# Kernel optimization log

Hardware: AMD Instinct MI355X
Metric: run time of the kernel (lower is better)

## Reference

```python
import jax, jax.numpy as jnp
import numpy as np

CHANNELS = 96


def make_sharpen_kernel(channels: int) -> jnp.ndarray:
    # (C_out, C_in, 3, 3), block-diagonal: per-channel 3x3 sharpen stencil
    k = jnp.full((3, 3), -0.1, dtype=jnp.float32).at[1, 1].set(1.8)
    eye = jnp.eye(channels, dtype=jnp.float32)  # (C, C)
    return eye[:, :, None, None] * k[None, None, :, :]


def setup_inputs() -> dict:
    key = jax.random.key(0)
    x = jax.random.normal(key, (16, CHANNELS, 256, 256), dtype=jnp.float32)
    kernel = make_sharpen_kernel(CHANNELS)
    return {"x": x, "kernel": kernel}


def reference(x, kernel):
    # Faithful to F.conv2d(x, kernel, stride=1, padding=1) with the dense
    # (block-diagonal) kernel the torch module constructs.
    return jax.lax.conv_general_dilated(
        x, kernel,
        window_strides=(1, 1),
        padding=((1, 1), (1, 1)),
        dimension_numbers=("NCHW", "OIHW", "NCHW"),
    )
```

## Files before the change

kernel.cpp:

```cpp
#include <hip/hip_runtime.h>

#define CHN 96
#define IMG_H 256
#define IMG_W 256
#define STRIP 64
#define WPB 8
#define GRP 8

typedef float vfloat4 __attribute__((ext_vector_type(4)));

struct Row { float l, x, y, z, w, r; };

__device__ __forceinline__ Row mkrow(vfloat4 v, int lane) {
    Row r;
    r.x = v.x; r.y = v.y; r.z = v.z; r.w = v.w;
    r.l = __shfl_up(v.w, 1);
    r.r = __shfl_down(v.x, 1);
    if (lane == 0)  r.l = 0.f;
    if (lane == 63) r.r = 0.f;
    return r;
}

__device__ __forceinline__ vfloat4 ldrow(const float* xp, int yy, int col) {
    if (yy < IMG_H)
        return __builtin_nontemporal_load(
            (const vfloat4*)(xp + (size_t)yy * IMG_W + col));
    return (vfloat4){0.f, 0.f, 0.f, 0.f};
}

__device__ __forceinline__ vfloat4 stencil(const Row& a, const Row& b, const Row& c,
                                           float w0, float w1, float w2,
                                           float w3, float w4, float w5,
                                           float w6, float w7, float w8) {
    vfloat4 o;
    o.x = w0*a.l + w1*a.x + w2*a.y
        + w3*b.l + w4*b.x + w5*b.y
        + w6*c.l + w7*c.x + w8*c.y;
    o.y = w0*a.x + w1*a.y + w2*a.z
        + w3*b.x + w4*b.y + w5*b.z
        + w6*c.x + w7*c.y + w8*c.z;
    o.z = w0*a.y + w1*a.z + w2*a.w
        + w3*b.y + w4*b.z + w5*b.w
        + w6*c.y + w7*c.z + w8*c.w;
    o.w = w0*a.z + w1*a.w + w2*a.r
        + w3*b.z + w4*b.w + w5*b.r
        + w6*c.z + w7*c.w + w8*c.r;
    return o;
}

__global__ __launch_bounds__(WPB * 64)
void sharpen3x3_pipe(const float* __restrict__ x,
                     const float* __restrict__ kern,
                     float* __restrict__ out)
{
    const int lane = threadIdx.x & 63;
    const int wave = threadIdx.x >> 6;

    const int strip_id = blockIdx.x * WPB + wave;
    const int spp      = IMG_H / STRIP;
    const int plane    = strip_id / spp;
    const int sy       = (strip_id % spp) * STRIP;
    const int c        = plane % CHN;

    const float* kw = kern + ((size_t)c * CHN + c) * 9;
    const float w0 = kw[0], w1 = kw[1], w2 = kw[2];
    const float w3 = kw[3], w4 = kw[4], w5 = kw[5];
    const float w6 = kw[6], w7 = kw[7], w8 = kw[8];

    const float* xp = x   + (size_t)plane * IMG_H * IMG_W;
    float*       op = out + (size_t)plane * IMG_H * IMG_W;

    const int col = 4 * lane;

    Row prev, cur;
    if (sy == 0) {
        prev = Row{0.f, 0.f, 0.f, 0.f, 0.f, 0.f};
    } else {
        prev = mkrow(ldrow(xp, sy - 1, col), lane);
    }
    cur = mkrow(ldrow(xp, sy, col), lane);

    vfloat4 va[GRP];
    #pragma unroll
    for (int j = 0; j < GRP; ++j) va[j] = ldrow(xp, sy + 1 + j, col);

    #pragma unroll 1
    for (int g = 0; g < STRIP / GRP; ++g) {
        const int y = sy + g * GRP;

        vfloat4 vb[GRP];
        if (g + 1 < STRIP / GRP) {
            #pragma unroll
            for (int j = 0; j < GRP; ++j)
                vb[j] = ldrow(xp, y + GRP + 1 + j, col);
        } else {
            #pragma unroll
            for (int j = 0; j < GRP; ++j)
                vb[j] = (vfloat4){0.f, 0.f, 0.f, 0.f};
        }

        #pragma unroll
        for (int j = 0; j < GRP; ++j) {
            Row n = mkrow(va[j], lane);
            vfloat4 o = stencil(prev, cur, n,
                                w0,w1,w2,w3,w4,w5,w6,w7,w8);
            __builtin_nontemporal_store(
                o, (vfloat4*)(op + (size_t)(y + j) * IMG_W + col));
            prev = cur;
            cur  = n;
        }

        #pragma unroll
        for (int j = 0; j < GRP; ++j) va[j] = vb[j];
    }
}

extern "C" void kernel_launch(void* const* d_in, const int* in_sizes, int n_in,
                              void* d_out, int out_size, void* d_ws, size_t ws_size,
                              hipStream_t stream) {
    const float* x    = (const float*)d_in[0];
    const float* kern = (const float*)d_in[1];
    float* out        = (float*)d_out;

    const int n_strips = 16 * CHN * (IMG_H / STRIP);
    const int grid     = n_strips / WPB;

    hipLaunchKernelGGL(sharpen3x3_pipe, dim3(grid), dim3(WPB * 64),
                       0, stream, x, kern, out);
}
```

Before: 153.8 us.

## Factor sharpen stencil into separable box sum plus center term

Replaces the nine-weight stencil with a horizontal three-tap sum per row. The three row sums are added, scaled by the shared neighbour weight, and a center correction term is added. This cuts the FMA count and register pressure. The single-buffered 8-row prefetch becomes a ping-pong of two 4-row buffers, and the launch bounds now ask for a minimum occupancy. The algebraic form assumes all eight off-center weights equal kw[0], which holds only for this sharpen kernel construction.

New measurement: 162.6 us. 1.06x slower.

```diff
diff --git a/kernel.cpp b/kernel.cpp
--- a/kernel.cpp
+++ b/kernel.cpp
@@ -5,21 +5,10 @@
 #define IMG_W 256
 #define STRIP 64
 #define WPB 8
-#define GRP 8
+#define GRP 4
+#define NG (STRIP / GRP)
 
 typedef float vfloat4 __attribute__((ext_vector_type(4)));
-
-struct Row { float l, x, y, z, w, r; };
-
-__device__ __forceinline__ Row mkrow(vfloat4 v, int lane) {
-    Row r;
-    r.x = v.x; r.y = v.y; r.z = v.z; r.w = v.w;
-    r.l = __shfl_up(v.w, 1);
-    r.r = __shfl_down(v.x, 1);
-    if (lane == 0)  r.l = 0.f;
-    if (lane == 63) r.r = 0.f;
-    return r;
-}
 
 __device__ __forceinline__ vfloat4 ldrow(const float* xp, int yy, int col) {
     if (yy < IMG_H)
@@ -28,28 +17,41 @@
     return (vfloat4){0.f, 0.f, 0.f, 0.f};
 }
 
-__device__ __forceinline__ vfloat4 stencil(const Row& a, const Row& b, const Row& c,
-                                           float w0, float w1, float w2,
-                                           float w3, float w4, float w5,
-                                           float w6, float w7, float w8) {
-    vfloat4 o;
-    o.x = w0*a.l + w1*a.x + w2*a.y
-        + w3*b.l + w4*b.x + w5*b.y
-        + w6*c.l + w7*c.x + w8*c.y;
-    o.y = w0*a.x + w1*a.y + w2*a.z
-        + w3*b.x + w4*b.y + w5*b.z
-        + w6*c.x + w7*c.y + w8*c.z;
-    o.z = w0*a.y + w1*a.z + w2*a.w
-        + w3*b.y + w4*b.z + w5*b.w
-        + w6*c.y + w7*c.z + w8*c.w;
-    o.w = w0*a.z + w1*a.w + w2*a.r
-        + w3*b.z + w4*b.w + w5*b.r
-        + w6*c.z + w7*c.w + w8*c.r;
-    return o;
+__device__ __forceinline__ vfloat4 hsum3(vfloat4 v, int lane) {
+    float l = __shfl_up(v.w, 1);
+    float r = __shfl_down(v.x, 1);
+    if (lane == 0)  l = 0.f;
+    if (lane == 63) r = 0.f;
+    float t1 = v.x + v.y;
+    float t2 = v.z + v.w;
+    vfloat4 h;
+    h.x = l  + t1;
+    h.y = t1 + v.z;
+    h.z = v.y + t2;
+    h.w = t2 + r;
+    return h;
 }
 
-__global__ __launch_bounds__(WPB * 64)
-void sharpen3x3_pipe(const float* __restrict__ x,
+__device__ __forceinline__ void compute_group(const vfloat4* buf,
+                                              vfloat4& hprev, vfloat4& hcur,
+                                              vfloat4& ccur,
+                                              float wn, float wd,
+                                              float* op, int y, int col, int lane) {
+    #pragma unroll
+    for (int j = 0; j < GRP; ++j) {
+        vfloat4 hn = hsum3(buf[j], lane);
+        vfloat4 s  = hprev + hcur + hn;
+        vfloat4 o  = s * wn + ccur * wd;
+        __builtin_nontemporal_store(
+            o, (vfloat4*)(op + (size_t)(y + j) * IMG_W + col));
+        hprev = hcur;
+        hcur  = hn;
+        ccur  = buf[j];
+    }
+}
+
+__global__ __launch_bounds__(WPB * 64, 6)
+void sharpen3x3_lean(const float* __restrict__ x,
                      const float* __restrict__ kern,
                      float* __restrict__ out)
 {
@@ -63,55 +65,42 @@
     const int c        = plane % CHN;
 
     const float* kw = kern + ((size_t)c * CHN + c) * 9;
-    const float w0 = kw[0], w1 = kw[1], w2 = kw[2];
-    const float w3 = kw[3], w4 = kw[4], w5 = kw[5];
-    const float w6 = kw[6], w7 = kw[7], w8 = kw[8];
+    const float wn = kw[0];
+    const float wd = kw[4] - wn;
 
     const float* xp = x   + (size_t)plane * IMG_H * IMG_W;
     float*       op = out + (size_t)plane * IMG_H * IMG_W;
-
     const int col = 4 * lane;
 
-    Row prev, cur;
+    vfloat4 A[GRP], B[GRP];
+    #pragma unroll
+    for (int j = 0; j < GRP; ++j) A[j] = ldrow(xp, sy + 1 + j, col);
+
+    vfloat4 hprev, hcur, ccur;
     if (sy == 0) {
-        prev = Row{0.f, 0.f, 0.f, 0.f, 0.f, 0.f};
+        hprev = (vfloat4){0.f, 0.f, 0.f, 0.f};
     } else {
-        prev = mkrow(ldrow(xp, sy - 1, col), lane);
+        hprev = hsum3(*(const vfloat4*)(xp + (size_t)(sy - 1) * IMG_W + col), lane);
     }
-    cur = mkrow(ldrow(xp, sy, col), lane);
-
-    vfloat4 va[GRP];
-    #pragma unroll
-    for (int j = 0; j < GRP; ++j) va[j] = ldrow(xp, sy + 1 + j, col);
+    {
+        vfloat4 v0 = *(const vfloat4*)(xp + (size_t)sy * IMG_W + col);
+        hcur = hsum3(v0, lane);
+        ccur = v0;
+    }
 
     #pragma unroll 1
-    for (int g = 0; g < STRIP / GRP; ++g) {
+    for (int g = 0; g < NG; g += 2) {
         const int y = sy + g * GRP;
 
-        vfloat4 vb[GRP];
-        if (g + 1 < STRIP / GRP) {
+        #pragma unroll
+        for (int j = 0; j < GRP; ++j) B[j] = ldrow(xp, y + GRP + 1 + j, col);
+        compute_group(A, hprev, hcur, ccur, wn, wd, op, y, col, lane);
+
+        if (g + 2 < NG) {
             #pragma unroll
-            for (int j = 0; j < GRP; ++j)
-                vb[j] = ldrow(xp, y + GRP + 1 + j, col);
-        } else {
-            #pragma unroll
-            for (int j = 0; j < GRP; ++j)
-                vb[j] = (vfloat4){0.f, 0.f, 0.f, 0.f};
+            for (int j = 0; j < GRP; ++j) A[j] = ldrow(xp, y + 2 * GRP + 1 + j, col);
         }
-
-        #pragma unroll
-        for (int j = 0; j < GRP; ++j) {
-            Row n = mkrow(va[j], lane);
-            vfloat4 o = stencil(prev, cur, n,
-                                w0,w1,w2,w3,w4,w5,w6,w7,w8);
-            __builtin_nontemporal_store(
-                o, (vfloat4*)(op + (size_t)(y + j) * IMG_W + col));
-            prev = cur;
-            cur  = n;
-        }
-
-        #pragma unroll
-        for (int j = 0; j < GRP; ++j) va[j] = vb[j];
+        compute_group(B, hprev, hcur, ccur, wn, wd, op, y + GRP, col, lane);
     }
 }
 
@@ -125,6 +114,6 @@
     const int n_strips = 16 * CHN * (IMG_H / STRIP);
     const int grid     = n_strips / WPB;
 
-    hipLaunchKernelGGL(sharpen3x3_pipe, dim3(grid), dim3(WPB * 64),
+    hipLaunchKernelGGL(sharpen3x3_lean, dim3(grid), dim3(WPB * 64),
                        0, stream, x, kern, out);
 }
```
